# Kernel optimization log

Measured on AMD Instinct MI355X. Metric: run time of the kernel, lower is better.

Reference implementation:

```python
import jax, jax.numpy as jnp
import numpy as np
from jax import lax

EPS = 0.1        # entropic regularization
MAX_ITER = 100   # Sinkhorn iteration budget
THRESH = 0.1     # early-stop threshold on err = mean_b sum_i |u - u_prev|
B, N, D = 16, 1024, 64


def setup_inputs() -> dict:
    key = jax.random.key(0)
    k1, k2 = jax.random.split(key)
    x = jax.random.normal(k1, (B, N, D), dtype=jnp.float32)
    y = jax.random.normal(k2, (B, N, D), dtype=jnp.float32)
    return {"x": x, "y": y}


def _lse(A):
    # Faithful to the original (unstabilized) lse: log(sum(exp(A)) + 1e-6)
    return jnp.log(jnp.exp(A).sum(-1) + 1e-6)


def _M(C, u, v):
    # (-C_ij + u_i + v_j) / eps
    return (-C + u[..., :, None] + v[..., None, :]) / EPS


def _cost_matrix(x, y):
    # (avoids materializing the [B, N, N, D] difference tensor; same math for p=2)
    x2 = (x * x).sum(-1)                         # [B, N]
    y2 = (y * y).sum(-1)                         # [B, N]
    xy = jnp.einsum('bid,bjd->bij', x, y)        # [B, N, N]
    return x2[..., :, None] + y2[..., None, :] - 2.0 * xy


def reference(x, y):
    x = jax.nn.softmax(x, axis=-1)
    y = jax.nn.softmax(y, axis=-1)
    C = _cost_matrix(x, y)                       # [B, N, N]
    n = x.shape[-2]
    log_mu = jnp.log(1.0 / n + 1e-8)             # mu = nu = uniform 1/n (scalar broadcast)
    u0 = jnp.zeros((x.shape[0], n), dtype=C.dtype)
    v0 = jnp.zeros_like(u0)

    def cond(carry):
        _, _, i, err = carry
        return jnp.logical_and(i < MAX_ITER, err >= THRESH)

    def body(carry):
        u, v, i, _ = carry
        u1 = u
        u = EPS * (log_mu - _lse(_M(C, u, v))) + u
        v = EPS * (log_mu - _lse(jnp.swapaxes(_M(C, u, v), -2, -1))) + v
        err = jnp.abs(u - u1).sum(-1).mean()
        return (u, v, i + 1, err)

    u, v, _, _ = lax.while_loop(
        cond, body, (u0, v0, jnp.int32(0), jnp.float32(jnp.inf)))

    pi = jnp.exp(_M(C, u, v))                    # transport plan [B, N, N]
    cost = (pi * C).sum((-2, -1))                # [B]
    return cost.mean()                           # reduction='mean'
```

## Files before the change

kernel.cpp:

```cpp
#include <hip/hip_runtime.h>
#include <hip/hip_bf16.h>
#include <math.h>

#define BATCH 16
#define NPTS 1024
#define DIM 64
#define EPSF 0.1f
#define INV_EPS 10.0f
#define MAX_ITER 100
#define THRESHF 0.1f
#define LSTRIDE 72

typedef _Float16 h8 __attribute__((ext_vector_type(8)));
typedef short short8v __attribute__((ext_vector_type(8)));
typedef float float4v __attribute__((ext_vector_type(4)));

#define ATOMIC_ST(p, v) \
  __hip_atomic_store((p), (v), __ATOMIC_RELAXED, __HIP_MEMORY_SCOPE_AGENT)
#define ATOMIC_LD(p) \
  __hip_atomic_load((p), __ATOMIC_RELAXED, __HIP_MEMORY_SCOPE_AGENT)

__device__ inline float waveSum(float x) {
#pragma unroll
  for (int off = 32; off; off >>= 1) x += __shfl_xor(x, off, 64);
  return x;
}
__device__ inline float waveMax(float x) {
#pragma unroll
  for (int off = 32; off; off >>= 1) x = fmaxf(x, __shfl_xor(x, off, 64));
  return x;
}

__global__ __launch_bounds__(256) void softmax_init(
    const float* __restrict__ x, const float* __restrict__ y,
    __hip_bfloat16* __restrict__ sxh, __hip_bfloat16* __restrict__ syh,
    float* __restrict__ x2, float* __restrict__ y2, float* __restrict__ errB,
    unsigned* __restrict__ flags, unsigned* __restrict__ doneCnt,
    float* __restrict__ costAcc) {
  int wv = (blockIdx.x * 256 + threadIdx.x) >> 6;
  int lane = threadIdx.x & 63;
#pragma unroll
  for (int rr = 0; rr < 8; rr++) {
    int row = wv * 8 + rr;
    const float* src;
    __hip_bfloat16* dst;
    float* ss;
    int r;
    if (row < BATCH * NPTS) {
      src = x; dst = sxh; ss = x2; r = row;
    } else {
      src = y; dst = syh; ss = y2; r = row - BATCH * NPTS;
    }
    float val = src[(size_t)r * DIM + lane];
    float m = waveMax(val);
    float e = expf(val - m);
    float s = waveSum(e);
    float p = e / s;
    dst[(size_t)r * DIM + lane] = (__hip_bfloat16)p;
    float sq = waveSum(p * p);
    if (lane == 0) ss[r] = sq;
  }
  if (blockIdx.x == 0) {
    for (int i = threadIdx.x; i < MAX_ITER * BATCH; i += 256) errB[i] = -1.0f;
    if (threadIdx.x < BATCH * 16) flags[threadIdx.x] = 0u;
    if (threadIdx.x == 0) { doneCnt[0] = 0u; costAcc[0] = 0.f; }
  }
}

__global__ __launch_bounds__(512, 1) void sinkhorn_fused(
    const __hip_bfloat16* __restrict__ sxh,
    const __hip_bfloat16* __restrict__ syh, const float* __restrict__ x2,
    const float* __restrict__ y2,
    float* __restrict__ partial,
    float* __restrict__ deltaPub,
    float* __restrict__ errB,
    unsigned* __restrict__ flags,
    unsigned* __restrict__ doneCnt, float* __restrict__ costAcc,
    float* __restrict__ out) {
  __shared__ __attribute__((aligned(16))) short xs[64 * LSTRIDE];
  __shared__ __attribute__((aligned(16))) short ys[2][64 * LSTRIDE];
  __shared__ __attribute__((aligned(16))) short os[2][64 * LSTRIDE];
  __shared__ __attribute__((aligned(16))) float wLDS[NPTS];
  __shared__ __attribute__((aligned(16))) float vLDS[NPTS];
  __shared__ __attribute__((aligned(16))) float colpart[8][NPTS];
  __shared__ float derr[8];
  __shared__ float errbL[BATCH];
  const int t = threadIdx.x;
  const int blk = blockIdx.x;
  const int wave = t >> 6, lane = t & 63;
  const int batch = (blk & 7) + 8 * (blk >> 7);
  const int kslot = (blk >> 3) & 15;
  const float log_mu = logf(1.0f / 1024.0f + 1e-8f);

  const int m = lane & 15, q = lane >> 4;
  const int g = lane >> 3, sub = lane & 7;
  const int sw = wave & 3, ts = wave >> 2;
  {
    int r = t >> 3, c = t & 7;
    *(short8v*)&xs[r * LSTRIDE + c * 8] = *(const short8v*)(
        (const short*)sxh + ((size_t)batch * NPTS + kslot * 64 + r) * DIM + c * 8);
  }
  __syncthreads();
  short8v a0 = *(const short8v*)&xs[(sw * 16 + m) * LSTRIDE + q * 8];
  short8v a1 = *(const short8v*)&xs[(sw * 16 + m) * LSTRIDE + 32 + q * 8];
  float4 x4 = *(const float4*)(x2 + (size_t)batch * NPTS + kslot * 64 + sw * 16 + q * 4);
  float xa[4] = {x4.x, x4.y, x4.z, x4.w};
  h8 ka[8], kb[8];
#pragma unroll
  for (int k = 0; k < 8; k++) {
    {
      int idx = t;
#pragma unroll
      for (int rep = 0; rep < 2; rep++, idx += 512) {
        int r = idx >> 3, c = idx & 7;
        *(short8v*)&ys[r >> 6][(r & 63) * LSTRIDE + c * 8] = *(const short8v*)(
            (const short*)syh + ((size_t)batch * NPTS + 128 * k + r) * DIM + c * 8);
      }
    }
    __syncthreads();
    const int jt = 2 * k + ts;
    float4v accv[4];
#pragma unroll
    for (int tj = 0; tj < 4; tj++) {
      short8v b0 = *(const short8v*)&ys[ts][(tj * 16 + m) * LSTRIDE + q * 8];
      short8v b1 = *(const short8v*)&ys[ts][(tj * 16 + m) * LSTRIDE + 32 + q * 8];
      float4v c = {0.f, 0.f, 0.f, 0.f};
      c = __builtin_amdgcn_mfma_f32_16x16x32_bf16(a0, b0, c, 0, 0, 0);
      c = __builtin_amdgcn_mfma_f32_16x16x32_bf16(a1, b1, c, 0, 0, 0);
      accv[tj] = c;
    }
#pragma unroll
    for (int tj = 0; tj < 4; tj++) {
      float y2v = y2[(size_t)batch * NPTS + jt * 64 + tj * 16 + m];
#pragma unroll
      for (int reg = 0; reg < 4; reg++) {
        float C = xa[reg] + y2v - 2.0f * accv[tj][reg];
        _Float16 kv = (_Float16)expf(-INV_EPS * C);
        os[ts][(sw * 16 + q * 4 + reg) * LSTRIDE + tj * 16 + m] = *(const short*)&kv;
      }
    }
    __syncthreads();
    {
      int e0 = (2 * k) & 7, e1 = (2 * k + 1) & 7;
      if (g == e0 || g == e1) {
        const short* srcp = (g == e0) ? &os[0][0] : &os[1][0];
#pragma unroll
        for (int rr = 0; rr < 8; rr++) {
          h8 v = *(const h8*)&srcp[(wave * 8 + rr) * LSTRIDE + sub * 8];
          if (k < 4) ka[rr] = v; else kb[rr] = v;
        }
      }
    }
    __syncthreads();
  }

  for (int j = t; j < NPTS; j += 512) { vLDS[j] = 0.f; wLDS[j] = 1.f; }
  __syncthreads();

  float u[8], uPrev[8];
#pragma unroll
  for (int r = 0; r < 8; r++) u[r] = 0.f;
  int it = 0;
  bool stopped = false;

  while (true) {
#pragma unroll
    for (int r = 0; r < 8; r++) uPrev[r] = u[r];
    const float4* w4 = (const float4*)wLDS;
    float wreg[16];
    *(float4*)&wreg[0]  = w4[2 * lane];
    *(float4*)&wreg[4]  = w4[2 * lane + 1];
    *(float4*)&wreg[8]  = w4[128 + 2 * lane];
    *(float4*)&wreg[12] = w4[128 + 2 * lane + 1];
    float colreg[16];
#pragma unroll
    for (int n = 0; n < 16; n++) colreg[n] = 0.f;
    float delta = 0.f;
#pragma unroll
    for (int rr = 0; rr < 8; rr++) {
      float kf[16];
#pragma unroll
      for (int n = 0; n < 8; n++) {
        kf[n] = (float)ka[rr][n];
        kf[8 + n] = (float)kb[rr][n];
      }
      float dot = 0.f;
#pragma unroll
      for (int n = 0; n < 16; n++) dot = fmaf(kf[n], wreg[n], dot);
      dot = waveSum(dot);
      float uo = u[rr];
      float s = expf(INV_EPS * uo) * dot;
      float un = EPSF * (log_mu - logf(s + 1e-6f)) + uo;
      delta += fabsf(un - uo);
      u[rr] = un;
      float ai = expf(INV_EPS * un);
#pragma unroll
      for (int n = 0; n < 16; n++) colreg[n] = fmaf(kf[n], ai, colreg[n]);
    }
    if (lane == 0) derr[wave] = delta;
    {
      float4* cp = (float4*)&colpart[wave][0];
      cp[2 * lane]       = make_float4(colreg[0], colreg[1], colreg[2], colreg[3]);
      cp[2 * lane + 1]   = make_float4(colreg[4], colreg[5], colreg[6], colreg[7]);
      cp[128 + 2 * lane] = make_float4(colreg[8], colreg[9], colreg[10], colreg[11]);
      cp[128 + 2 * lane + 1] = make_float4(colreg[12], colreg[13], colreg[14], colreg[15]);
    }
    __syncthreads();
    float* pp = partial + ((size_t)(it & 1) * BATCH + batch) * (NPTS * 16);
#pragma unroll
    for (int rep = 0; rep < 2; rep++) {
      int j = t + rep * 512;
      float s = 0.f;
#pragma unroll
      for (int w = 0; w < 8; w++) s += colpart[w][j];
      ATOMIC_ST(&pp[kslot * NPTS + j], s);
    }
    if (t == 0) {
      float e = 0.f;
#pragma unroll
      for (int w = 0; w < 8; w++) e += derr[w];
      ATOMIC_ST(&deltaPub[((it & 1) * BATCH + batch) * 16 + kslot], e);
    }
    __syncthreads();
    if (t == 0) ATOMIC_ST(&flags[batch * 16 + kslot], (unsigned)(it + 1));
    if (t < 16) {
      while (ATOMIC_LD(&flags[batch * 16 + t]) < (unsigned)(it + 1))
        __builtin_amdgcn_s_sleep(1);
    }
    __syncthreads();
    if (kslot == 0 && t == 0) {
      const float* dp = deltaPub + ((it & 1) * BATCH + batch) * 16;
      float e = 0.f;
#pragma unroll
      for (int k = 0; k < 16; k++) e += ATOMIC_LD((float*)&dp[k]);
      ATOMIC_ST(&errB[it * BATCH + batch], e);
    }
    float ps0[16], ps1[16];
#pragma unroll
    for (int k = 0; k < 16; k++) ps0[k] = ATOMIC_LD(&pp[k * NPTS + t]);
#pragma unroll
    for (int k = 0; k < 16; k++) ps1[k] = ATOMIC_LD(&pp[k * NPTS + t + 512]);
    if (it >= 1) {
      if (t < BATCH) {
        float v;
        while ((v = ATOMIC_LD(&errB[(it - 1) * BATCH + t])) < 0.f)
          __builtin_amdgcn_s_sleep(1);
        errbL[t] = v;
      }
      __syncthreads();
      float errv = 0.f;
#pragma unroll
      for (int k = 0; k < BATCH; k++) errv += errbL[k];
      if (errv * (1.0f / (float)BATCH) < THRESHF) {
#pragma unroll
        for (int r = 0; r < 8; r++) u[r] = uPrev[r];
        stopped = true;
        break;
      }
    }
#pragma unroll
    for (int rep = 0; rep < 2; rep++) {
      int j = t + rep * 512;
      const float* ps = rep ? ps1 : ps0;
      float cs = 0.f;
#pragma unroll
      for (int k = 0; k < 16; k++) cs += ps[k];
      float vo = vLDS[j];
      float s = expf(INV_EPS * vo) * cs;
      float vn = EPSF * (log_mu - logf(s + 1e-6f)) + vo;
      vLDS[j] = vn;
      wLDS[j] = expf(INV_EPS * vn);
    }
    it++;
    if (it >= MAX_ITER) break;
    __syncthreads();
  }
  (void)stopped;

  {
    __syncthreads();
    const float4* w4 = (const float4*)wLDS;
    float wreg[16];
    *(float4*)&wreg[0]  = w4[2 * lane];
    *(float4*)&wreg[4]  = w4[2 * lane + 1];
    *(float4*)&wreg[8]  = w4[128 + 2 * lane];
    *(float4*)&wreg[12] = w4[128 + 2 * lane + 1];
    float csum = 0.f;
#pragma unroll
    for (int rr = 0; rr < 8; rr++) {
      float kf[16];
#pragma unroll
      for (int n = 0; n < 8; n++) {
        kf[n] = (float)ka[rr][n];
        kf[8 + n] = (float)kb[rr][n];
      }
      float ai = expf(INV_EPS * u[rr]);
#pragma unroll
      for (int n = 0; n < 16; n++) {
        if (kf[n] > 0.f)
          csum += ai * wreg[n] * kf[n] * (-EPSF * logf(kf[n]));
      }
    }
    csum = waveSum(csum);
    if (lane == 0) derr[wave] = csum;
    __syncthreads();
    if (t == 0) {
      float cs = 0.f;
#pragma unroll
      for (int w = 0; w < 8; w++) cs += derr[w];
      atomicAdd(costAcc, cs);
      unsigned old = __hip_atomic_fetch_add(doneCnt, 1u, __ATOMIC_ACQ_REL,
                                            __HIP_MEMORY_SCOPE_AGENT);
      if (old == 255u) {
        float total = __hip_atomic_load(costAcc, __ATOMIC_ACQUIRE,
                                        __HIP_MEMORY_SCOPE_AGENT);
        out[0] = total * (1.0f / (float)BATCH);
      }
    }
  }
}

extern "C" void kernel_launch(void* const* d_in, const int* in_sizes, int n_in,
                              void* d_out, int out_size, void* d_ws,
                              size_t ws_size, hipStream_t stream) {
  (void)in_sizes; (void)n_in; (void)out_size; (void)ws_size;
  const float* x = (const float*)d_in[0];
  const float* y = (const float*)d_in[1];
  float* out = (float*)d_out;

  char* ws = (char*)d_ws;
  size_t off = 0;
  auto alloc = [&](size_t nbytes) -> void* {
    void* p = (void*)(ws + off);
    off = (off + nbytes + 255) & ~(size_t)255;
    return p;
  };
  __hip_bfloat16* sxh = (__hip_bfloat16*)alloc((size_t)BATCH * NPTS * DIM * 2);
  __hip_bfloat16* syh = (__hip_bfloat16*)alloc((size_t)BATCH * NPTS * DIM * 2);
  float* x2 = (float*)alloc((size_t)BATCH * NPTS * 4);
  float* y2 = (float*)alloc((size_t)BATCH * NPTS * 4);
  float* partial = (float*)alloc((size_t)2 * BATCH * NPTS * 16 * 4);
  float* deltaPub = (float*)alloc((size_t)2 * BATCH * 16 * 4);
  float* errB = (float*)alloc((size_t)MAX_ITER * BATCH * 4);
  unsigned* flags = (unsigned*)alloc((size_t)BATCH * 16 * 4);
  unsigned* doneCnt = (unsigned*)alloc(64);
  float* costAcc = (float*)alloc(64);

  softmax_init<<<dim3(1024), 256, 0, stream>>>(x, y, sxh, syh, x2, y2, errB,
                                               flags, doneCnt, costAcc);
  void* args[] = {&sxh, &syh, &x2, &y2, &partial, &deltaPub,
                  &errB, &flags, &doneCnt, &costAcc, &out};
  hipLaunchCooperativeKernel((void*)sinkhorn_fused, dim3(256), dim3(512), args,
                             0, stream);
}
```

Before: 141.5 us.

## Reduce column partials with global atomic adds into triple-buffered colsum

Each of the 16 k-slot blocks per batch now adds its column partial sums atomically into a single per-batch column-sum buffer, instead of writing its own slice that every block later reads back 16 times. The buffer rotates over three slots, and each block clears its share of the slot two iterations ahead. This cuts global reads and per-thread reduction work in the cross-block exchange. Spin loops also drop s_sleep to poll with lower latency. The cost is atomic contention in L2 and float summation order that now varies from run to run.

```diff
diff --git a/kernel.cpp b/kernel.cpp
--- a/kernel.cpp
+++ b/kernel.cpp
@@ -34,9 +34,10 @@
 __global__ __launch_bounds__(256) void softmax_init(
     const float* __restrict__ x, const float* __restrict__ y,
     __hip_bfloat16* __restrict__ sxh, __hip_bfloat16* __restrict__ syh,
-    float* __restrict__ x2, float* __restrict__ y2, float* __restrict__ errB,
-    unsigned* __restrict__ flags, unsigned* __restrict__ doneCnt,
-    float* __restrict__ costAcc) {
+    float* __restrict__ x2, float* __restrict__ y2,
+    float* __restrict__ colsum,
+    float* __restrict__ errB, unsigned* __restrict__ flags,
+    unsigned* __restrict__ doneCnt, float* __restrict__ costAcc) {
   int wv = (blockIdx.x * 256 + threadIdx.x) >> 6;
   int lane = threadIdx.x & 63;
 #pragma unroll
@@ -60,18 +61,18 @@
     float sq = waveSum(p * p);
     if (lane == 0) ss[r] = sq;
   }
-  if (blockIdx.x == 0) {
-    for (int i = threadIdx.x; i < MAX_ITER * BATCH; i += 256) errB[i] = -1.0f;
-    if (threadIdx.x < BATCH * 16) flags[threadIdx.x] = 0u;
-    if (threadIdx.x == 0) { doneCnt[0] = 0u; costAcc[0] = 0.f; }
-  }
+  int gtid = blockIdx.x * 256 + threadIdx.x;
+  if (gtid < 3 * BATCH * NPTS) colsum[gtid] = 0.f;
+  if (gtid < MAX_ITER * BATCH) errB[gtid] = -1.0f;
+  if (gtid < BATCH * 16) flags[gtid] = 0u;
+  if (gtid == 0) { doneCnt[0] = 0u; costAcc[0] = 0.f; }
 }
 
 __global__ __launch_bounds__(512, 1) void sinkhorn_fused(
     const __hip_bfloat16* __restrict__ sxh,
     const __hip_bfloat16* __restrict__ syh, const float* __restrict__ x2,
     const float* __restrict__ y2,
-    float* __restrict__ partial,
+    float* __restrict__ colsum,
     float* __restrict__ deltaPub,
     float* __restrict__ errB,
     unsigned* __restrict__ flags,
@@ -161,7 +162,6 @@
 #pragma unroll
   for (int r = 0; r < 8; r++) u[r] = 0.f;
   int it = 0;
-  bool stopped = false;
 
   while (true) {
 #pragma unroll
@@ -206,14 +206,14 @@
       cp[128 + 2 * lane + 1] = make_float4(colreg[12], colreg[13], colreg[14], colreg[15]);
     }
     __syncthreads();
-    float* pp = partial + ((size_t)(it & 1) * BATCH + batch) * (NPTS * 16);
+    float* cs = colsum + ((size_t)(it % 3) * BATCH + batch) * NPTS;
 #pragma unroll
     for (int rep = 0; rep < 2; rep++) {
       int j = t + rep * 512;
       float s = 0.f;
 #pragma unroll
       for (int w = 0; w < 8; w++) s += colpart[w][j];
-      ATOMIC_ST(&pp[kslot * NPTS + j], s);
+      unsafeAtomicAdd(&cs[j], s);
     }
     if (t == 0) {
       float e = 0.f;
@@ -224,10 +224,14 @@
     __syncthreads();
     if (t == 0) ATOMIC_ST(&flags[batch * 16 + kslot], (unsigned)(it + 1));
     if (t < 16) {
-      while (ATOMIC_LD(&flags[batch * 16 + t]) < (unsigned)(it + 1))
-        __builtin_amdgcn_s_sleep(1);
-    }
-    __syncthreads();
+      while (ATOMIC_LD(&flags[batch * 16 + t]) < (unsigned)(it + 1)) {}
+    }
+    __syncthreads();
+    float cs0 = ATOMIC_LD(&cs[t]);
+    float cs1 = ATOMIC_LD(&cs[t + 512]);
+    if (t < 64)
+      ATOMIC_ST(&colsum[((size_t)((it + 2) % 3) * BATCH + batch) * NPTS +
+                        kslot * 64 + t], 0.f);
     if (kslot == 0 && t == 0) {
       const float* dp = deltaPub + ((it & 1) * BATCH + batch) * 16;
       float e = 0.f;
@@ -235,16 +239,10 @@
       for (int k = 0; k < 16; k++) e += ATOMIC_LD((float*)&dp[k]);
       ATOMIC_ST(&errB[it * BATCH + batch], e);
     }
-    float ps0[16], ps1[16];
-#pragma unroll
-    for (int k = 0; k < 16; k++) ps0[k] = ATOMIC_LD(&pp[k * NPTS + t]);
-#pragma unroll
-    for (int k = 0; k < 16; k++) ps1[k] = ATOMIC_LD(&pp[k * NPTS + t + 512]);
     if (it >= 1) {
       if (t < BATCH) {
         float v;
-        while ((v = ATOMIC_LD(&errB[(it - 1) * BATCH + t])) < 0.f)
-          __builtin_amdgcn_s_sleep(1);
+        while ((v = ATOMIC_LD(&errB[(it - 1) * BATCH + t])) < 0.f) {}
         errbL[t] = v;
       }
       __syncthreads();
@@ -254,28 +252,25 @@
       if (errv * (1.0f / (float)BATCH) < THRESHF) {
 #pragma unroll
         for (int r = 0; r < 8; r++) u[r] = uPrev[r];
-        stopped = true;
         break;
       }
     }
-#pragma unroll
-    for (int rep = 0; rep < 2; rep++) {
-      int j = t + rep * 512;
-      const float* ps = rep ? ps1 : ps0;
-      float cs = 0.f;
-#pragma unroll
-      for (int k = 0; k < 16; k++) cs += ps[k];
-      float vo = vLDS[j];
-      float s = expf(INV_EPS * vo) * cs;
+    {
+      float vo = vLDS[t];
+      float s = expf(INV_EPS * vo) * cs0;
       float vn = EPSF * (log_mu - logf(s + 1e-6f)) + vo;
-      vLDS[j] = vn;
-      wLDS[j] = expf(INV_EPS * vn);
+      vLDS[t] = vn;
+      wLDS[t] = expf(INV_EPS * vn);
+      float vo1 = vLDS[t + 512];
+      float s1 = expf(INV_EPS * vo1) * cs1;
+      float vn1 = EPSF * (log_mu - logf(s1 + 1e-6f)) + vo1;
+      vLDS[t + 512] = vn1;
+      wLDS[t + 512] = expf(INV_EPS * vn1);
     }
     it++;
     if (it >= MAX_ITER) break;
     __syncthreads();
   }
-  (void)stopped;
 
   {
     __syncthreads();
@@ -339,16 +334,16 @@
   __hip_bfloat16* syh = (__hip_bfloat16*)alloc((size_t)BATCH * NPTS * DIM * 2);
   float* x2 = (float*)alloc((size_t)BATCH * NPTS * 4);
   float* y2 = (float*)alloc((size_t)BATCH * NPTS * 4);
-  float* partial = (float*)alloc((size_t)2 * BATCH * NPTS * 16 * 4);
+  float* colsum = (float*)alloc((size_t)3 * BATCH * NPTS * 4);
   float* deltaPub = (float*)alloc((size_t)2 * BATCH * 16 * 4);
   float* errB = (float*)alloc((size_t)MAX_ITER * BATCH * 4);
   unsigned* flags = (unsigned*)alloc((size_t)BATCH * 16 * 4);
   unsigned* doneCnt = (unsigned*)alloc(64);
   float* costAcc = (float*)alloc(64);
 
-  softmax_init<<<dim3(1024), 256, 0, stream>>>(x, y, sxh, syh, x2, y2, errB,
-                                               flags, doneCnt, costAcc);
-  void* args[] = {&sxh, &syh, &x2, &y2, &partial, &deltaPub,
+  softmax_init<<<dim3(1024), 256, 0, stream>>>(x, y, sxh, syh, x2, y2, colsum,
+                                               errB, flags, doneCnt, costAcc);
+  void* args[] = {&sxh, &syh, &x2, &y2, &colsum, &deltaPub,
                   &errB, &flags, &doneCnt, &costAcc, &out};
   hipLaunchCooperativeKernel((void*)sinkhorn_fused, dim3(256), dim3(512), args,
                              0, stream);
```

After: 138.2 us. -2.3%, faster.
